# Performance work log

Hardware: AMD Instinct MI355X
Metric: run time of the kernel (lower is better)

Reference implementation:

```python
import jax, jax.numpy as jnp
import numpy as np

HIDDEN = 4096
N_HEADS = 32
N_KV_HEADS = 8
HEAD_DIM = HIDDEN // N_HEADS  # 128
N_GROUPS = N_HEADS // N_KV_HEADS  # 4
ROPE_THETA = 10000.0
NEG_INF = -1e9


def fake_quant(x):
    """Symmetric per-tensor int8 fake quantization (quantize -> dequantize)."""
    scale = jnp.maximum(jnp.max(jnp.abs(x)) / 127.0, 1e-8)
    return jnp.clip(jnp.round(x / scale), -127.0, 127.0) * scale


def q_linear(x, W):
    # torch Linear: y = x @ W.T ; both operands fake-quantized (dequant-inline GEMM)
    return jnp.einsum('bsh,oh->bso', fake_quant(x), fake_quant(W))


def rope_cos_sin(position_ids, head_dim, dtype):
    inv_freq = 1.0 / (ROPE_THETA ** (jnp.arange(0, head_dim, 2, dtype=jnp.float32) / head_dim))
    freqs = position_ids.astype(jnp.float32)[..., None] * inv_freq  # [b, s, hd/2]
    emb = jnp.concatenate([freqs, freqs], axis=-1)                   # [b, s, hd]
    return jnp.cos(emb).astype(dtype), jnp.sin(emb).astype(dtype)


def rotate_half(x):
    x1, x2 = jnp.split(x, 2, axis=-1)
    return jnp.concatenate([-x2, x1], axis=-1)


def setup_inputs() -> dict:
    key = jax.random.key(0)
    ks = jax.random.split(key, 6)
    b, s = 2, 1024
    hidden_states = jax.random.normal(ks[0], (b, s, HIDDEN), dtype=jnp.float32)
    # additive causal mask [b, 1, q, kv]
    causal = jnp.where(jnp.tril(jnp.ones((s, s), dtype=bool)), 0.0, NEG_INF).astype(jnp.float32)
    attention_mask = jnp.broadcast_to(causal[None, None], (b, 1, s, s))
    position_ids = jnp.broadcast_to(jnp.arange(s, dtype=jnp.int64)[None, :], (b, s))
    winit = 1.0 / np.sqrt(HIDDEN)
    Wq = jax.random.normal(ks[1], (HIDDEN, HIDDEN), dtype=jnp.float32) * winit
    Wk = jax.random.normal(ks[2], (N_KV_HEADS * HEAD_DIM, HIDDEN), dtype=jnp.float32) * winit
    Wv = jax.random.normal(ks[3], (N_KV_HEADS * HEAD_DIM, HIDDEN), dtype=jnp.float32) * winit
    Wo = jax.random.normal(ks[4], (HIDDEN, HIDDEN), dtype=jnp.float32) * winit
    return {"hidden_states": hidden_states, "attention_mask": attention_mask,
            "position_ids": position_ids, "Wq": Wq, "Wk": Wk, "Wv": Wv, "Wo": Wo}


def reference(hidden_states, attention_mask, position_ids, Wq, Wk, Wv, Wo):
    b, s, _ = hidden_states.shape
    dtype = hidden_states.dtype

    # quantized QKV projections
    q = q_linear(hidden_states, Wq).reshape(b, s, N_HEADS, HEAD_DIM).transpose(0, 2, 1, 3)
    k = q_linear(hidden_states, Wk).reshape(b, s, N_KV_HEADS, HEAD_DIM).transpose(0, 2, 1, 3)
    v = q_linear(hidden_states, Wv).reshape(b, s, N_KV_HEADS, HEAD_DIM).transpose(0, 2, 1, 3)

    # RoPE
    cos, sin = rope_cos_sin(position_ids, HEAD_DIM, dtype)  # [b, s, hd]
    cos, sin = cos[:, None], sin[:, None]                   # broadcast over heads
    q = q * cos + rotate_half(q) * sin
    k = k * cos + rotate_half(k) * sin

    # GQA: repeat kv heads
    k = jnp.repeat(k, N_GROUPS, axis=1)  # [b, H, s, hd]
    v = jnp.repeat(v, N_GROUPS, axis=1)

    # quantized QK^T (per-tensor fake quant on both operands)
    attn = jnp.einsum('bhqd,bhkd->bhqk', fake_quant(q), fake_quant(k)) / jnp.sqrt(
        jnp.asarray(HEAD_DIM, dtype=jnp.float32)).astype(dtype)
    attn = attn + attention_mask
    attn = jax.nn.softmax(attn.astype(jnp.float32), axis=-1).astype(dtype)
    # attention_dropout = 0.0 (inference)

    # quantized AV matmul
    out = jnp.einsum('bhqk,bhkd->bhqd', fake_quant(attn), fake_quant(v))
    out = out.transpose(0, 2, 1, 3).reshape(b, s, HIDDEN)
    out = q_linear(out, Wo)
    return out
```

## Files before the change

kernel.cpp:

```cpp
#include <hip/hip_runtime.h>
#include <math.h>

#define B_ 2
#define S_ 1024
#define HID 4096
#define NH 32
#define NKV 8
#define HD 128
#define LOG2E 1.44269504088896340736f

typedef short s16x8 __attribute__((ext_vector_type(8)));
typedef float f32x4 __attribute__((ext_vector_type(4)));
typedef int i32x4 __attribute__((ext_vector_type(4)));
typedef unsigned short u16;
typedef u16 u16x4 __attribute__((ext_vector_type(4)));
typedef signed char s8;

__device__ __forceinline__ f32x4 mfma16(s16x8 a, s16x8 b, f32x4 c) {
  return __builtin_amdgcn_mfma_f32_16x16x32_bf16(a, b, c, 0, 0, 0);
}
__device__ __forceinline__ i32x4 mfma_i8(i32x4 a, i32x4 b, i32x4 c) {
  return __builtin_amdgcn_mfma_i32_16x16x64_i8(a, b, c, 0, 0, 0);
}
__device__ __forceinline__ u16 f2bf(float f) {
  union { float f; unsigned u; } v; v.f = f;
  return (u16)(v.u >> 16);
}
__device__ __forceinline__ float get_scale(const unsigned* sc, int slot) {
  return fmaxf(__uint_as_float(sc[slot]) / 127.0f, 1e-8f);
}
__device__ __forceinline__ int q127(float x, float s) {
  return (int)fminf(fmaxf(rintf(x / s), -127.f), 127.f);
}
__device__ __forceinline__ unsigned pack4(float4 v, float s) {
  return (q127(v.x, s) & 255) | ((q127(v.y, s) & 255) << 8) |
         ((q127(v.z, s) & 255) << 16) | ((q127(v.w, s) & 255) << 24);
}
__device__ __forceinline__ float max4(float4 v) {
  return fmaxf(fmaxf(fabsf(v.x), fabsf(v.y)), fmaxf(fabsf(v.z), fabsf(v.w)));
}
__device__ __forceinline__ void gload16(const void* g, void* l) {
  __builtin_amdgcn_global_load_lds(
      (const __attribute__((address_space(1))) unsigned*)g,
      (__attribute__((address_space(3))) unsigned*)l, 16, 0, 0);
}
__device__ __forceinline__ void atomic_absmax(unsigned* out, float m, int lane) {
  #pragma unroll
  for (int o = 32; o >= 1; o >>= 1) m = fmaxf(m, __shfl_xor(m, o));
  if (lane == 0) atomicMax(out, __float_as_uint(m));
}

#define SB_() __builtin_amdgcn_sched_barrier(0)
#define PBAR() do { SB_(); __builtin_amdgcn_s_barrier(); SB_(); } while (0)
#define VM6() do { SB_(); asm volatile("s_waitcnt vmcnt(6)" ::: "memory"); } while (0)
#define VM0() do { SB_(); asm volatile("s_waitcnt vmcnt(0)" ::: "memory"); } while (0)

__device__ __forceinline__ void tensor_pick(int blk, int& r, int& b0, int& nb) {
  if (blk < 342)       { r = 0; b0 = 0;    nb = 342; }
  else if (blk < 1024) { r = 1; b0 = 342;  nb = 682; }
  else if (blk < 1195) { r = 2; b0 = 1024; nb = 171; }
  else if (blk < 1366) { r = 3; b0 = 1195; nb = 171; }
  else                 { r = 4; b0 = 1366; nb = 682; }
}

__global__ void absmax5_k(const float4* __restrict__ p0, const float4* __restrict__ p1,
                          const float4* __restrict__ p2, const float4* __restrict__ p3,
                          const float4* __restrict__ p4, unsigned* __restrict__ sc) {
  int r, b0, nb;
  tensor_pick(blockIdx.x, r, b0, nb);
  const float4* x; int n4;
  if (r == 0)      { x = p0; n4 = B_ * S_ * HID / 4; }
  else if (r == 1) { x = p1; n4 = HID * HID / 4; }
  else if (r == 2) { x = p2; n4 = NKV * HD * HID / 4; }
  else if (r == 3) { x = p3; n4 = NKV * HD * HID / 4; }
  else             { x = p4; n4 = HID * HID / 4; }
  const int stride = nb * 256;
  int i = (blockIdx.x - b0) * 256 + threadIdx.x;
  float m0 = 0.f, m1 = 0.f, m2 = 0.f, m3 = 0.f;
  for (; i + 3 * stride < n4; i += 4 * stride) {
    float4 v0 = x[i], v1 = x[i + stride], v2 = x[i + 2 * stride], v3 = x[i + 3 * stride];
    m0 = fmaxf(m0, max4(v0)); m1 = fmaxf(m1, max4(v1));
    m2 = fmaxf(m2, max4(v2)); m3 = fmaxf(m3, max4(v3));
  }
  for (; i < n4; i += stride) m0 = fmaxf(m0, max4(x[i]));
  float m = fmaxf(fmaxf(m0, m1), fmaxf(m2, m3));
  atomic_absmax(sc + r, m, threadIdx.x & 63);
}

__global__ void quant5_k(const float4* __restrict__ p0, const float4* __restrict__ p1,
                         const float4* __restrict__ p2, const float4* __restrict__ p3,
                         const float4* __restrict__ p4,
                         unsigned* __restrict__ y0, unsigned* __restrict__ y1,
                         unsigned* __restrict__ y2, unsigned* __restrict__ y3,
                         unsigned* __restrict__ y4, const unsigned* __restrict__ sc) {
  int r, b0, nb;
  tensor_pick(blockIdx.x, r, b0, nb);
  const float4* x; unsigned* y; int n4;
  if (r == 0)      { x = p0; y = y0; n4 = B_ * S_ * HID / 4; }
  else if (r == 1) { x = p1; y = y1; n4 = HID * HID / 4; }
  else if (r == 2) { x = p2; y = y2; n4 = NKV * HD * HID / 4; }
  else if (r == 3) { x = p3; y = y3; n4 = NKV * HD * HID / 4; }
  else             { x = p4; y = y4; n4 = HID * HID / 4; }
  float s = get_scale(sc, r);
  const int stride = nb * 256;
  int i = (blockIdx.x - b0) * 256 + threadIdx.x;
  for (; i + 3 * stride < n4; i += 4 * stride) {
    float4 v0 = x[i], v1 = x[i + stride], v2 = x[i + 2 * stride], v3 = x[i + 3 * stride];
    y[i] = pack4(v0, s);
    y[i + stride] = pack4(v1, s);
    y[i + 2 * stride] = pack4(v2, s);
    y[i + 3 * stride] = pack4(v3, s);
  }
  for (; i < n4; i += stride) y[i] = pack4(x[i], s);
}

__global__ void quant_k(const float4* __restrict__ x, unsigned* __restrict__ y, int n4,
                        const unsigned* __restrict__ sc, int slot) {
  float s = get_scale(sc, slot);
  int stride = gridDim.x * blockDim.x;
  int i = blockIdx.x * blockDim.x + threadIdx.x;
  for (; i + 3 * stride < n4; i += 4 * stride) {
    float4 v0 = x[i], v1 = x[i + stride], v2 = x[i + 2 * stride], v3 = x[i + 3 * stride];
    y[i] = pack4(v0, s);
    y[i + stride] = pack4(v1, s);
    y[i + 2 * stride] = pack4(v2, s);
    y[i + 3 * stride] = pack4(v3, s);
  }
  for (; i < n4; i += stride) y[i] = pack4(x[i], s);
}

__global__ void add_k(const float4* __restrict__ p0, const float4* __restrict__ p1,
                      float4* __restrict__ out, int n4) {
  int stride = gridDim.x * blockDim.x;
  int i = blockIdx.x * blockDim.x + threadIdx.x;
  for (; i + stride < n4; i += 2 * stride) {
    float4 a0 = p0[i], b0 = p1[i], a1 = p0[i + stride], b1 = p1[i + stride];
    out[i] = make_float4(a0.x + b0.x, a0.y + b0.y, a0.z + b0.z, a0.w + b0.w);
    out[i + stride] = make_float4(a1.x + b1.x, a1.y + b1.y, a1.z + b1.z, a1.w + b1.w);
  }
  for (; i < n4; i += stride) {
    float4 a = p0[i], b = p1[i];
    out[i] = make_float4(a.x + b.x, a.y + b.y, a.z + b.z, a.w + b.w);
  }
}

__device__ __forceinline__ void rdA(const s8* slot, int wm, int lr, int lg,
                                    i32x4 af[4][2]) {
  #pragma unroll
  for (int mi = 0; mi < 4; ++mi) {
    int row = wm * 64 + mi * 16 + lr;
    const char* base = (const char*)slot + row * 128;
    int sw = (row & 7) << 4;
    #pragma unroll
    for (int ks = 0; ks < 2; ++ks)
      af[mi][ks] = *(const i32x4*)(base + ((ks * 64 + lg * 16) ^ sw));
  }
}
__device__ __forceinline__ void rdB(const s8* slot, int wn, int lr, int lg,
                                    i32x4 bf[2][2]) {
  #pragma unroll
  for (int ni = 0; ni < 2; ++ni) {
    int row = wn * 32 + ni * 16 + lr;
    const char* base = (const char*)slot + row * 128;
    int sw = (row & 7) << 4;
    #pragma unroll
    for (int ks = 0; ks < 2; ++ks)
      bf[ni][ks] = *(const i32x4*)(base + ((ks * 64 + lg * 16) ^ sw));
  }
}
template <int PM, int PN>
__device__ __forceinline__ void mfma_phase(i32x4 (&acc)[2][2][4][2],
                                           const i32x4 (&af)[4][2],
                                           const i32x4 (&bf)[2][2]) {
  __builtin_amdgcn_s_setprio(1);
  #pragma unroll
  for (int mi = 0; mi < 4; ++mi)
    #pragma unroll
    for (int ni = 0; ni < 2; ++ni)
      #pragma unroll
      for (int ks = 0; ks < 2; ++ks)
        acc[PM][PN][mi][ni] = mfma_i8(af[mi][ks], bf[ni][ks], acc[PM][PN][mi][ni]);
  __builtin_amdgcn_s_setprio(0);
}

__device__ void gemm256(const s8* __restrict__ A, const s8* __restrict__ Bm,
                        float* __restrict__ C, int Ncols, int m0, int n0,
                        int k0, int nkt, float scale, unsigned* omax, s8* S) {
  const int tid = threadIdx.x;
  const int wave = tid >> 6, lane = tid & 63;
  const int lr = lane & 15, lg = lane >> 4;
  const int wm = wave >> 2, wn = wave & 3;
  s8* SA00 = S;          s8* SA01 = S + 16384;
  s8* SB00 = S + 32768;  s8* SB01 = S + 49152;
  s8* SA10 = S + 65536;  s8* SA11 = S + 81920;
  s8* SB10 = S + 98304;  s8* SB11 = S + 114688;
  const int r0 = tid >> 3;
  const int ce = ((tid & 7) * 16) ^ ((r0 & 7) << 4);
  const s8* pa0 = A + (size_t)(m0 + r0) * HID + k0 + ce;
  const s8* pa1 = pa0 + (size_t)128 * HID;
  const s8* pb0 = Bm + (size_t)(n0 + r0) * HID + k0 + ce;
  const s8* pb1 = pb0 + (size_t)128 * HID;
  const int wdst = wave * 1024;
  i32x4 acc[2][2][4][2] = {};
  i32x4 af[4][2], bf[2][2];

  auto STG = [&](const s8* p, s8* slot, int tcol) {
    const s8* g = p + tcol * 128;
    gload16(g, slot + wdst);
    gload16(g + (size_t)64 * HID, slot + 8192 + wdst);
  };

  STG(pa0, SA00, 0); STG(pb0, SB00, 0); STG(pa1, SA01, 0); STG(pb1, SB01, 0);
  STG(pa0, SA10, 1); STG(pb1, SB11, 1); STG(pa1, SA11, 1);
  VM6(); PBAR();

  #pragma unroll 1
  for (int t = 0; t < nkt; t += 2) {
    const bool g2 = t + 2 < nkt, g3 = t + 3 < nkt;
    rdA(SA00, wm, lr, lg, af); rdB(SB00, wn, lr, lg, bf);
    STG(pb0, SB10, t + 1);
    PBAR(); mfma_phase<0, 0>(acc, af, bf); PBAR();
    rdB(SB01, wn, lr, lg, bf);
    if (g2) STG(pa0, SA00, t + 2);
    PBAR(); mfma_phase<0, 1>(acc, af, bf); PBAR();
    rdA(SA01, wm, lr, lg, af);
    if (g2) STG(pb1, SB01, t + 2);
    PBAR(); mfma_phase<1, 1>(acc, af, bf); PBAR();
    rdB(SB00, wn, lr, lg, bf);
    if (g2) STG(pa1, SA01, t + 2);
    PBAR(); mfma_phase<1, 0>(acc, af, bf);
    if (g2) { VM6(); } else { VM0(); }
    PBAR();
    rdA(SA10, wm, lr, lg, af); rdB(SB10, wn, lr, lg, bf);
    if (g2) STG(pb0, SB00, t + 2);
    PBAR(); mfma_phase<0, 0>(acc, af, bf); PBAR();
    rdB(SB11, wn, lr, lg, bf);
    if (g3) STG(pa0, SA10, t + 3);
    PBAR(); mfma_phase<0, 1>(acc, af, bf); PBAR();
    rdA(SA11, wm, lr, lg, af);
    if (g3) STG(pb1, SB11, t + 3);
    PBAR(); mfma_phase<1, 1>(acc, af, bf); PBAR();
    rdB(SB10, wn, lr, lg, bf);
    if (g3) STG(pa1, SA11, t + 3);
    PBAR(); mfma_phase<1, 0>(acc, af, bf); VM6(); PBAR();
  }

  float gm = 0.f;
  #pragma unroll
  for (int mh = 0; mh < 2; ++mh)
    #pragma unroll
    for (int nh = 0; nh < 2; ++nh)
      #pragma unroll
      for (int mi = 0; mi < 4; ++mi)
        #pragma unroll
        for (int ni = 0; ni < 2; ++ni) {
          size_t rbase = (size_t)(m0 + mh * 128 + wm * 64 + mi * 16 + lg * 4);
          int cb = n0 + nh * 128 + wn * 32 + ni * 16 + lr;
          #pragma unroll
          for (int r = 0; r < 4; ++r) {
            float v = (float)acc[mh][nh][mi][ni][r] * scale;
            gm = fmaxf(gm, fabsf(v));
            C[(rbase + r) * (size_t)Ncols + cb] = v;
          }
        }
  if (omax) atomic_absmax(omax, gm, lane);
}

__global__ __launch_bounds__(512, 1) void gemm_qkv8(
    const s8* __restrict__ Xq, const s8* __restrict__ Wqb,
    const s8* __restrict__ Wkb, const s8* __restrict__ Wvb,
    float* __restrict__ qf, float* __restrict__ kf, float* __restrict__ vf,
    const unsigned* __restrict__ sc, unsigned* __restrict__ vmax) {
  extern __shared__ __align__(16) s8 S[];
  int raw = blockIdx.x;
  int wg = (raw & 7) * 24 + (raw >> 3);
  int bx = wg & 7, by = wg >> 3;
  const s8* Bm; float* C; int Ncols, n0, sslot; unsigned* om = nullptr;
  if (by < 16)      { Bm = Wqb; C = qf; Ncols = HID;      n0 = by * 256;        sslot = 1; }
  else if (by < 20) { Bm = Wkb; C = kf; Ncols = NKV * HD; n0 = (by - 16) * 256; sslot = 2; }
  else              { Bm = Wvb; C = vf; Ncols = NKV * HD; n0 = (by - 20) * 256; sslot = 3; om = vmax; }
  float scale = get_scale(sc, 0) * get_scale(sc, sslot);
  gemm256(Xq, Bm, C, Ncols, bx * 256, n0, 0, 32, scale, om, S);
}

__global__ __launch_bounds__(512, 1) void gemm_o8(
    const s8* __restrict__ A, const s8* __restrict__ Bm,
    float* __restrict__ P0, float* __restrict__ P1,
    const unsigned* __restrict__ sc) {
  extern __shared__ __align__(16) s8 S[];
  int raw = blockIdx.x;
  int wg = (raw & 7) * 32 + (raw >> 3);
  int tile = wg >> 1, half = wg & 1;
  int by = tile & 15, bx = tile >> 4;
  float scale = get_scale(sc, 8) * get_scale(sc, 4);
  gemm256(A, Bm, half ? P1 : P0, HID, bx * 256, by * 256, half * 2048, 16,
          scale, nullptr, S);
}

__global__ void rope_tab_k(float2* __restrict__ tab) {
  int i = blockIdx.x * 256 + threadIdx.x;
  int pos = i >> 6, d = i & 63;
  float inv = exp2f((float)d * (-13.287712379549449f / 64.0f));
  float ang = (float)pos * inv;
  tab[i] = make_float2(cosf(ang), sinf(ang));
}

__global__ void rope2_k(float* __restrict__ qf, float* __restrict__ kf,
                        unsigned* __restrict__ sc, const float2* __restrict__ tab) {
  int reg = blockIdx.y;
  float* q = reg ? kf : qf;
  int nheads = reg ? NKV : NH;
  unsigned* om = sc + (reg ? 6 : 5);
  int total = B_ * S_ * nheads * 16;
  int stride = gridDim.x * blockDim.x;
  float m = 0.f;
  for (int i = blockIdx.x * blockDim.x + threadIdx.x; i < total; i += stride) {
    int g = i & 15;
    int h = (i >> 4) % nheads;
    int bs = i / (16 * nheads);
    int pos = bs & (S_ - 1);
    size_t base = ((size_t)bs * nheads + h) * HD + g * 4;
    float4 x1 = *(float4*)(q + base);
    float4 x2 = *(float4*)(q + base + 64);
    const float4* t = (const float4*)(tab + ((size_t)pos << 6) + g * 4);
    float4 t0 = t[0], t1 = t[1];
    float4 o1, o2;
    o1.x = x1.x * t0.x - x2.x * t0.y;  o2.x = x2.x * t0.x + x1.x * t0.y;
    o1.y = x1.y * t0.z - x2.y * t0.w;  o2.y = x2.y * t0.z + x1.y * t0.w;
    o1.z = x1.z * t1.x - x2.z * t1.y;  o2.z = x2.z * t1.x + x1.z * t1.y;
    o1.w = x1.w * t1.z - x2.w * t1.w;  o2.w = x2.w * t1.z + x1.w * t1.w;
    *(float4*)(q + base) = o1;
    *(float4*)(q + base + 64) = o2;
    m = fmaxf(m, fmaxf(max4(o1), max4(o2)));
  }
  atomic_absmax(om, m, threadIdx.x & 63);
}

__global__ void quantqk_k(const float4* __restrict__ qf, const float4* __restrict__ kf,
                          u16x4* __restrict__ qq, u16x4* __restrict__ kq,
                          const unsigned* __restrict__ sc) {
  int reg = blockIdx.y;
  const float4* x = reg ? kf : qf;
  u16x4* y = reg ? kq : qq;
  int n4 = reg ? (B_ * S_ * NKV * HD / 4) : (B_ * S_ * HID / 4);
  float s = get_scale(sc, reg ? 6 : 5);
  int stride = gridDim.x * blockDim.x;
  for (int i = blockIdx.x * blockDim.x + threadIdx.x; i < n4; i += stride) {
    float4 v = x[i];
    u16x4 o;
    o[0] = f2bf(fminf(fmaxf(rintf(v.x / s), -127.f), 127.f));
    o[1] = f2bf(fminf(fmaxf(rintf(v.y / s), -127.f), 127.f));
    o[2] = f2bf(fminf(fmaxf(rintf(v.z / s), -127.f), 127.f));
    o[3] = f2bf(fminf(fmaxf(rintf(v.w / s), -127.f), 127.f));
    y[i] = o;
  }
}

__global__ __launch_bounds__(256) void vquant_t_k(const float* __restrict__ vf,
                                                  unsigned* __restrict__ vtw,
                                                  const unsigned* __restrict__ sc) {
  __shared__ u16 Ls[64 * 132];
  float s = get_scale(sc, 7);
  int st = blockIdx.x & 15, kvh = (blockIdx.x >> 4) & 7, b = blockIdx.x >> 7;
  int s0 = st * 64;
  #pragma unroll
  for (int i = 0; i < 8; ++i) {
    int o = i * 256 + threadIdx.x;
    int sr = o >> 5, c4 = o & 31;
    float4 v = *(const float4*)(vf + ((size_t)(b * S_ + s0 + sr)) * (NKV * HD) +
                                kvh * HD + c4 * 4);
    u16x4 w;
    w[0] = f2bf(fminf(fmaxf(rintf(v.x / s), -127.f), 127.f));
    w[1] = f2bf(fminf(fmaxf(rintf(v.y / s), -127.f), 127.f));
    w[2] = f2bf(fminf(fmaxf(rintf(v.z / s), -127.f), 127.f));
    w[3] = f2bf(fminf(fmaxf(rintf(v.w / s), -127.f), 127.f));
    *(u16x4*)(Ls + sr * 132 + c4 * 4) = w;
  }
  __syncthreads();
  #pragma unroll
  for (int i = 0; i < 16; ++i) {
    int o = i * 256 + threadIdx.x;
    int d = o >> 5, sj = o & 31;
    unsigned lo = Ls[(sj * 2) * 132 + d], hi = Ls[(sj * 2 + 1) * 132 + d];
    vtw[(((size_t)(b * NKV + kvh) * HD + d) << 9) + st * 32 + sj] = lo | (hi << 16);
  }
}

__global__ __launch_bounds__(512) void attn_k(
    const u16* __restrict__ Q, const u16* __restrict__ Kq, const u16* __restrict__ Vt,
    float* __restrict__ O, const unsigned* __restrict__ sc, unsigned* __restrict__ omax) {
  __shared__ __align__(16) u16 Ks[2][64 * 128];
  __shared__ __align__(16) u16 Vs[2][128 * 64];
  __shared__ __align__(16) u16 Ps[128 * 64];
  const int tid = threadIdx.x;
  const int wave = tid >> 6, lane = tid & 63;
  const int lr = lane & 15, lg = lane >> 4;
  const int raw = blockIdx.x;
  const int xcd = raw & 7, j = raw >> 3;
  const int grp = xcd + 8 * (j >> 4);
  const int within = j & 15;
  const int b = grp >> 3, kvh = grp & 7;
  const int h = kvh * 4 + (within >> 2);
  const int qp = within & 3;
  const float sq = get_scale(sc, 5), sk = get_scale(sc, 6), sv = get_scale(sc, 7);
  const float c2 = sq * sk * 0.08838834764831845f * LOG2E;
  const float M0 = 32.0f;
  const int k_rin = lane >> 4;
  const int k_cb0 = (lane & 15) * 16;
  const int v_rin = lane >> 3;
  const int v_cb = ((lane & 7) * 16) ^ ((v_rin & 7) << 4);
  float gmax = 0.f;

  auto stageK = [&](int buf, int kt) {
    #pragma unroll
    for (int i = 0; i < 2; ++i) {
      int ch = wave * 2 + i;
      int row = ch * 4 + k_rin;
      int cb = k_cb0 ^ ((row & 7) << 4);
      gload16(Kq + (size_t)(b * S_ + kt * 64 + row) * (NKV * HD) + kvh * HD + (cb >> 1),
              Ks[buf] + ch * 512);
    }
  };
  auto stageV = [&](int buf, int kt) {
    #pragma unroll
    for (int i = 0; i < 2; ++i) {
      int ch = wave * 2 + i;
      int vrow = ch * 8 + v_rin;
      gload16(Vt + ((size_t)(b * NKV + kvh) * HD + vrow) * S_ + kt * 64 + (v_cb >> 1),
              Vs[buf] + ch * 512);
    }
  };

  for (int pi = 0; pi < 2; ++pi) {
    const int qt = pi ? 7 - qp : qp;
    const int q0 = qt * 128;
    const int nkt = 2 * (qt + 1);
    const int qwmin = q0 + wave * 16;
    s16x8 aq[4];
    {
      const u16* qp_ = Q + (size_t)(b * S_ + q0 + wave * 16 + lr) * HID + h * HD + lg * 8;
      #pragma unroll
      for (int ks = 0; ks < 4; ++ks) aq[ks] = *(const s16x8*)(qp_ + ks * 32);
    }
    float ll[4] = {0.f, 0.f, 0.f, 0.f};

    stageK(0, 0);
    __syncthreads();
    for (int kt = 0; kt < nkt; ++kt) {
      const int p = kt & 1;
      if (kt < nkt - 1) stageK(p ^ 1, kt + 1);
      f32x4 sacc[4] = {};
      __builtin_amdgcn_s_setprio(1);
      #pragma unroll
      for (int ks = 0; ks < 4; ++ks)
        #pragma unroll
        for (int n = 0; n < 4; ++n) {
          int row = n * 16 + lr;
          s16x8 bk = *(const s16x8*)((const char*)Ks[p] + row * 256 +
                                     ((ks * 64 + lg * 16) ^ ((row & 7) << 4)));
          sacc[n] = mfma16(aq[ks], bk, sacc[n]);
        }
      __builtin_amdgcn_s_setprio(0);
      if (kt * 64 + 63 <= qwmin) {
        #pragma unroll
        for (int r = 0; r < 4; ++r)
          #pragma unroll
          for (int n = 0; n < 4; ++n)
            ll[r] += exp2f(fmaf(sacc[n][r], c2, -M0));
      } else {
        #pragma unroll
        for (int r = 0; r < 4; ++r) {
          int qg = qwmin + lg * 4 + r;
          #pragma unroll
          for (int n = 0; n < 4; ++n) {
            int kg = kt * 64 + n * 16 + lr;
            float e = exp2f(fmaf(sacc[n][r], c2, -M0));
            ll[r] += (kg <= qg) ? e : 0.f;
          }
        }
      }
      __syncthreads();
    }
    float bias[4];
    #pragma unroll
    for (int r = 0; r < 4; ++r) {
      float l = ll[r];
      #pragma unroll
      for (int o = 8; o >= 1; o >>= 1) l += __shfl_xor(l, o);
      bias[r] = 6.9886846867721655f - __log2f(l) - M0;
    }

    f32x4 oacc[8] = {};
    stageK(0, 0); stageV(0, 0);
    __syncthreads();
    for (int kt = 0; kt < nkt; ++kt) {
      const int p = kt & 1;
      if (kt < nkt - 1) { stageK(p ^ 1, kt + 1); stageV(p ^ 1, kt + 1); }
      f32x4 sacc[4] = {};
      __builtin_amdgcn_s_setprio(1);
      #pragma unroll
      for (int ks = 0; ks < 4; ++ks)
        #pragma unroll
        for (int n = 0; n < 4; ++n) {
          int row = n * 16 + lr;
          s16x8 bk = *(const s16x8*)((const char*)Ks[p] + row * 256 +
                                     ((ks * 64 + lg * 16) ^ ((row & 7) << 4)));
          sacc[n] = mfma16(aq[ks], bk, sacc[n]);
        }
      __builtin_amdgcn_s_setprio(0);
      if (kt * 64 + 63 <= qwmin) {
        #pragma unroll
        for (int r = 0; r < 4; ++r) {
          int prow = wave * 16 + lg * 4 + r;
          #pragma unroll
          for (int n = 0; n < 4; ++n) {
            float p127 = rintf(exp2f(fmaf(sacc[n][r], c2, bias[r])));
            int col = n * 16 + lr;
            *(u16*)((char*)Ps + prow * 128 + ((col * 2) ^ ((prow & 7) << 4))) = f2bf(p127);
          }
        }
      } else {
        #pragma unroll
        for (int r = 0; r < 4; ++r) {
          int prow = wave * 16 + lg * 4 + r;
          int qg = qwmin + lg * 4 + r;
          #pragma unroll
          for (int n = 0; n < 4; ++n) {
            int kg = kt * 64 + n * 16 + lr;
            float a = fmaf(sacc[n][r], c2, bias[r]);
            float p127 = (kg <= qg) ? rintf(exp2f(a)) : 0.f;
            int col = n * 16 + lr;
            *(u16*)((char*)Ps + prow * 128 + ((col * 2) ^ ((prow & 7) << 4))) = f2bf(p127);
          }
        }
      }
      __builtin_amdgcn_s_setprio(1);
      #pragma unroll
      for (int ks = 0; ks < 2; ++ks) {
        int prow = wave * 16 + lr;
        s16x8 ap = *(const s16x8*)((const char*)Ps + prow * 128 +
                                   ((ks * 64 + lg * 16) ^ ((prow & 7) << 4)));
        #pragma unroll
        for (int n = 0; n < 8; ++n) {
          int vrow = n * 16 + lr;
          s16x8 bv = *(const s16x8*)((const char*)Vs[p] + vrow * 128 +
                                     ((ks * 64 + lg * 16) ^ ((vrow & 7) << 4)));
          oacc[n] = mfma16(ap, bv, oacc[n]);
        }
      }
      __builtin_amdgcn_s_setprio(0);
      __syncthreads();
    }
    const float pvs = sv * (1.0f / 127.0f);
    #pragma unroll
    for (int n = 0; n < 8; ++n)
      #pragma unroll
      for (int r = 0; r < 4; ++r) {
        float v = oacc[n][r] * pvs;
        gmax = fmaxf(gmax, fabsf(v));
        O[(size_t)(b * S_ + q0 + wave * 16 + lg * 4 + r) * HID + h * HD + n * 16 + lr] = v;
      }
  }
  atomic_absmax(omax, gmax, lane);
}

extern "C" void kernel_launch(void* const* d_in, const int* in_sizes, int n_in,
                              void* d_out, int out_size, void* d_ws, size_t ws_size,
                              hipStream_t stream) {
  const float* hs = (const float*)d_in[0];
  const float* Wq = (const float*)d_in[3];
  const float* Wk = (const float*)d_in[4];
  const float* Wv = (const float*)d_in[5];
  const float* Wo = (const float*)d_in[6];
  float* out = (float*)d_out;
  char* ws = (char*)d_ws;

  unsigned* sc = (unsigned*)ws;
  size_t off = 256;
  s8* Xq = (s8*)(ws + off); off += (size_t)B_ * S_ * HID;
  size_t wqb_off = off;
  s8* Wqb = (s8*)(ws + off); off += (size_t)HID * HID;
  s8* Wkb = (s8*)(ws + off); off += (size_t)NKV * HD * HID;
  s8* Wvb = (s8*)(ws + off); off += (size_t)NKV * HD * HID;
  s8* Wob = (s8*)(ws + off); off += (size_t)HID * HID;
  size_t qf_off = off;
  float* qf = (float*)(ws + off); off += (size_t)B_ * S_ * HID * 4;
  size_t kf_off = off;
  float* kf = (float*)(ws + off); off += (size_t)B_ * S_ * NKV * HD * 4;
  float* vf = (float*)(ws + off); off += (size_t)B_ * S_ * NKV * HD * 4;
  u16* qq = (u16*)(ws + off); off += (size_t)B_ * S_ * HID * 2;
  u16* kq = (u16*)(ws + off); off += (size_t)B_ * S_ * NKV * HD * 2;
  u16* vt = (u16*)(ws + off); off += (size_t)B_ * S_ * NKV * HD * 2;
  float2* tab = (float2*)(ws + off); off += (size_t)S_ * 64 * 8;
  float* attnf = (float*)(ws + qf_off);
  s8* attnq = (s8*)(ws + wqb_off);
  float* P0 = (float*)(ws + qf_off);
  float* P1 = (float*)(ws + kf_off);

  hipFuncSetAttribute((const void*)gemm_qkv8,
                      hipFuncAttributeMaxDynamicSharedMemorySize, 131072);
  hipFuncSetAttribute((const void*)gemm_o8,
                      hipFuncAttributeMaxDynamicSharedMemorySize, 131072);

  hipMemsetAsync(sc, 0, 64, stream);

  dim3 blk(256);
  absmax5_k<<<2048, blk, 0, stream>>>(
      (const float4*)hs, (const float4*)Wq, (const float4*)Wk,
      (const float4*)Wv, (const float4*)Wo, sc);
  quant5_k<<<2048, blk, 0, stream>>>(
      (const float4*)hs, (const float4*)Wq, (const float4*)Wk,
      (const float4*)Wv, (const float4*)Wo,
      (unsigned*)Xq, (unsigned*)Wqb, (unsigned*)Wkb, (unsigned*)Wvb,
      (unsigned*)Wob, sc);
  rope_tab_k<<<256, blk, 0, stream>>>(tab);

  gemm_qkv8<<<192, 512, 131072, stream>>>(Xq, Wqb, Wkb, Wvb, qf, kf, vf, sc, sc + 7);

  rope2_k<<<dim3(512, 2), blk, 0, stream>>>(qf, kf, sc, tab);
  quantqk_k<<<dim3(512, 2), blk, 0, stream>>>((const float4*)qf, (const float4*)kf,
                                              (u16x4*)qq, (u16x4*)kq, sc);
  vquant_t_k<<<256, blk, 0, stream>>>(vf, (unsigned*)vt, sc);

  attn_k<<<256, 512, 0, stream>>>(qq, kq, vt, attnf, sc, sc + 8);

  quant_k<<<2048, blk, 0, stream>>>((const float4*)attnf, (unsigned*)attnq,
                                    B_ * S_ * HID / 4, sc, 8);
  gemm_o8<<<256, 512, 131072, stream>>>(attnq, Wob, P0, P1, sc);
  add_k<<<2048, blk, 0, stream>>>((const float4*)P0, (const float4*)P1,
                                  (float4*)out, B_ * S_ * HID / 4);
}
```

Baseline: 459.8 us.

## Store quantized Q/K as int8 and use int8 MFMA for QK^T in attention

Q and K are now quantized to packed int8 instead of bf16-encoded integers. The attention kernel stages int8 K tiles, which halves the LDS footprint and the global load per tile, and computes QK^T with the 16x16x64 int8 MFMA, using half as many instructions per tile. The quant kernel's loop is unrolled by two. The P1 partial buffer is moved to its own workspace region because the smaller qq/kq layout changes the offsets, which uses more workspace memory.

```diff
diff --git a/kernel.cpp b/kernel.cpp
--- a/kernel.cpp
+++ b/kernel.cpp
@@ -337,23 +337,21 @@
 }
 
 __global__ void quantqk_k(const float4* __restrict__ qf, const float4* __restrict__ kf,
-                          u16x4* __restrict__ qq, u16x4* __restrict__ kq,
+                          unsigned* __restrict__ qq, unsigned* __restrict__ kq,
                           const unsigned* __restrict__ sc) {
   int reg = blockIdx.y;
   const float4* x = reg ? kf : qf;
-  u16x4* y = reg ? kq : qq;
+  unsigned* y = reg ? kq : qq;
   int n4 = reg ? (B_ * S_ * NKV * HD / 4) : (B_ * S_ * HID / 4);
   float s = get_scale(sc, reg ? 6 : 5);
   int stride = gridDim.x * blockDim.x;
-  for (int i = blockIdx.x * blockDim.x + threadIdx.x; i < n4; i += stride) {
-    float4 v = x[i];
-    u16x4 o;
-    o[0] = f2bf(fminf(fmaxf(rintf(v.x / s), -127.f), 127.f));
-    o[1] = f2bf(fminf(fmaxf(rintf(v.y / s), -127.f), 127.f));
-    o[2] = f2bf(fminf(fmaxf(rintf(v.z / s), -127.f), 127.f));
-    o[3] = f2bf(fminf(fmaxf(rintf(v.w / s), -127.f), 127.f));
-    y[i] = o;
-  }
+  int i = blockIdx.x * blockDim.x + threadIdx.x;
+  for (; i + stride < n4; i += 2 * stride) {
+    float4 v0 = x[i], v1 = x[i + stride];
+    y[i] = pack4(v0, s);
+    y[i + stride] = pack4(v1, s);
+  }
+  for (; i < n4; i += stride) y[i] = pack4(x[i], s);
 }
 
 __global__ __launch_bounds__(256) void vquant_t_k(const float* __restrict__ vf,
@@ -387,9 +385,9 @@
 }
 
 __global__ __launch_bounds__(512) void attn_k(
-    const u16* __restrict__ Q, const u16* __restrict__ Kq, const u16* __restrict__ Vt,
+    const s8* __restrict__ Q, const s8* __restrict__ Kq, const u16* __restrict__ Vt,
     float* __restrict__ O, const unsigned* __restrict__ sc, unsigned* __restrict__ omax) {
-  __shared__ __align__(16) u16 Ks[2][64 * 128];
+  __shared__ __align__(16) s8 Ks[2][64 * 128];
   __shared__ __align__(16) u16 Vs[2][128 * 64];
   __shared__ __align__(16) u16 Ps[128 * 64];
   const int tid = threadIdx.x;
@@ -405,21 +403,15 @@
   const float sq = get_scale(sc, 5), sk = get_scale(sc, 6), sv = get_scale(sc, 7);
   const float c2 = sq * sk * 0.08838834764831845f * LOG2E;
   const float M0 = 32.0f;
-  const int k_rin = lane >> 4;
-  const int k_cb0 = (lane & 15) * 16;
+  const int k_row = tid >> 3;
+  const int k_cb = ((tid & 7) * 16) ^ ((k_row & 7) << 4);
   const int v_rin = lane >> 3;
   const int v_cb = ((lane & 7) * 16) ^ ((v_rin & 7) << 4);
   float gmax = 0.f;
 
   auto stageK = [&](int buf, int kt) {
-    #pragma unroll
-    for (int i = 0; i < 2; ++i) {
-      int ch = wave * 2 + i;
-      int row = ch * 4 + k_rin;
-      int cb = k_cb0 ^ ((row & 7) << 4);
-      gload16(Kq + (size_t)(b * S_ + kt * 64 + row) * (NKV * HD) + kvh * HD + (cb >> 1),
-              Ks[buf] + ch * 512);
-    }
+    gload16(Kq + (size_t)(b * S_ + kt * 64 + k_row) * (NKV * HD) + kvh * HD + k_cb,
+            Ks[buf] + wave * 1024);
   };
   auto stageV = [&](int buf, int kt) {
     #pragma unroll
@@ -436,11 +428,11 @@
     const int q0 = qt * 128;
     const int nkt = 2 * (qt + 1);
     const int qwmin = q0 + wave * 16;
-    s16x8 aq[4];
+    i32x4 aq[2];
     {
-      const u16* qp_ = Q + (size_t)(b * S_ + q0 + wave * 16 + lr) * HID + h * HD + lg * 8;
-      #pragma unroll
-      for (int ks = 0; ks < 4; ++ks) aq[ks] = *(const s16x8*)(qp_ + ks * 32);
+      const s8* qp_ = Q + (size_t)(b * S_ + q0 + wave * 16 + lr) * HID + h * HD + lg * 16;
+      aq[0] = *(const i32x4*)(qp_);
+      aq[1] = *(const i32x4*)(qp_ + 64);
     }
     float ll[4] = {0.f, 0.f, 0.f, 0.f};
 
@@ -449,16 +441,16 @@
     for (int kt = 0; kt < nkt; ++kt) {
       const int p = kt & 1;
       if (kt < nkt - 1) stageK(p ^ 1, kt + 1);
-      f32x4 sacc[4] = {};
+      i32x4 sacc[4] = {};
       __builtin_amdgcn_s_setprio(1);
       #pragma unroll
-      for (int ks = 0; ks < 4; ++ks)
+      for (int ks = 0; ks < 2; ++ks)
         #pragma unroll
         for (int n = 0; n < 4; ++n) {
           int row = n * 16 + lr;
-          s16x8 bk = *(const s16x8*)((const char*)Ks[p] + row * 256 +
+          i32x4 bk = *(const i32x4*)((const char*)Ks[p] + row * 128 +
                                      ((ks * 64 + lg * 16) ^ ((row & 7) << 4)));
-          sacc[n] = mfma16(aq[ks], bk, sacc[n]);
+          sacc[n] = mfma_i8(aq[ks], bk, sacc[n]);
         }
       __builtin_amdgcn_s_setprio(0);
       if (kt * 64 + 63 <= qwmin) {
@@ -466,7 +458,7 @@
         for (int r = 0; r < 4; ++r)
           #pragma unroll
           for (int n = 0; n < 4; ++n)
-            ll[r] += exp2f(fmaf(sacc[n][r], c2, -M0));
+            ll[r] += exp2f(fmaf((float)sacc[n][r], c2, -M0));
       } else {
         #pragma unroll
         for (int r = 0; r < 4; ++r) {
@@ -474,7 +466,7 @@
           #pragma unroll
           for (int n = 0; n < 4; ++n) {
             int kg = kt * 64 + n * 16 + lr;
-            float e = exp2f(fmaf(sacc[n][r], c2, -M0));
+            float e = exp2f(fmaf((float)sacc[n][r], c2, -M0));
             ll[r] += (kg <= qg) ? e : 0.f;
           }
         }
@@ -496,16 +488,16 @@
     for (int kt = 0; kt < nkt; ++kt) {
       const int p = kt & 1;
       if (kt < nkt - 1) { stageK(p ^ 1, kt + 1); stageV(p ^ 1, kt + 1); }
-      f32x4 sacc[4] = {};
+      i32x4 sacc[4] = {};
       __builtin_amdgcn_s_setprio(1);
       #pragma unroll
-      for (int ks = 0; ks < 4; ++ks)
+      for (int ks = 0; ks < 2; ++ks)
         #pragma unroll
         for (int n = 0; n < 4; ++n) {
           int row = n * 16 + lr;
-          s16x8 bk = *(const s16x8*)((const char*)Ks[p] + row * 256 +
+          i32x4 bk = *(const i32x4*)((const char*)Ks[p] + row * 128 +
                                      ((ks * 64 + lg * 16) ^ ((row & 7) << 4)));
-          sacc[n] = mfma16(aq[ks], bk, sacc[n]);
+          sacc[n] = mfma_i8(aq[ks], bk, sacc[n]);
         }
       __builtin_amdgcn_s_setprio(0);
       if (kt * 64 + 63 <= qwmin) {
@@ -514,7 +506,7 @@
           int prow = wave * 16 + lg * 4 + r;
           #pragma unroll
           for (int n = 0; n < 4; ++n) {
-            float p127 = rintf(exp2f(fmaf(sacc[n][r], c2, bias[r])));
+            float p127 = rintf(exp2f(fmaf((float)sacc[n][r], c2, bias[r])));
             int col = n * 16 + lr;
             *(u16*)((char*)Ps + prow * 128 + ((col * 2) ^ ((prow & 7) << 4))) = f2bf(p127);
           }
@@ -527,7 +519,7 @@
           #pragma unroll
           for (int n = 0; n < 4; ++n) {
             int kg = kt * 64 + n * 16 + lr;
-            float a = fmaf(sacc[n][r], c2, bias[r]);
+            float a = fmaf((float)sacc[n][r], c2, bias[r]);
             float p127 = (kg <= qg) ? rintf(exp2f(a)) : 0.f;
             int col = n * 16 + lr;
             *(u16*)((char*)Ps + prow * 128 + ((col * 2) ^ ((prow & 7) << 4))) = f2bf(p127);
@@ -585,17 +577,16 @@
   s8* Wob = (s8*)(ws + off); off += (size_t)HID * HID;
   size_t qf_off = off;
   float* qf = (float*)(ws + off); off += (size_t)B_ * S_ * HID * 4;
-  size_t kf_off = off;
   float* kf = (float*)(ws + off); off += (size_t)B_ * S_ * NKV * HD * 4;
   float* vf = (float*)(ws + off); off += (size_t)B_ * S_ * NKV * HD * 4;
-  u16* qq = (u16*)(ws + off); off += (size_t)B_ * S_ * HID * 2;
-  u16* kq = (u16*)(ws + off); off += (size_t)B_ * S_ * NKV * HD * 2;
+  s8* qq = (s8*)(ws + off); off += (size_t)B_ * S_ * HID;
+  s8* kq = (s8*)(ws + off); off += (size_t)B_ * S_ * NKV * HD;
   u16* vt = (u16*)(ws + off); off += (size_t)B_ * S_ * NKV * HD * 2;
   float2* tab = (float2*)(ws + off); off += (size_t)S_ * 64 * 8;
+  float* P1 = (float*)(ws + off); off += (size_t)B_ * S_ * HID * 4;
   float* attnf = (float*)(ws + qf_off);
   s8* attnq = (s8*)(ws + wqb_off);
   float* P0 = (float*)(ws + qf_off);
-  float* P1 = (float*)(ws + kf_off);
 
   hipFuncSetAttribute((const void*)gemm_qkv8,
                       hipFuncAttributeMaxDynamicSharedMemorySize, 131072);
@@ -619,7 +610,7 @@
 
   rope2_k<<<dim3(512, 2), blk, 0, stream>>>(qf, kf, sc, tab);
   quantqk_k<<<dim3(512, 2), blk, 0, stream>>>((const float4*)qf, (const float4*)kf,
-                                              (u16x4*)qq, (u16x4*)kq, sc);
+                                              (unsigned*)qq, (unsigned*)kq, sc);
   vquant_t_k<<<256, blk, 0, stream>>>(vf, (unsigned*)vt, sc);
 
   attn_k<<<256, 512, 0, stream>>>(qq, kq, vt, attnf, sc, sc + 8);
```

Measured after the change: 449.9 us. 1.02x faster.
